# Kernel tuning notes

Measured on AMD Instinct MI355X. Metric: run time of the kernel, lower is better.

## Reference

```python
import jax, jax.numpy as jnp
import numpy as np

BASE_ALPHA = 0.05
NUM_ITER = 2
EPS = 1e-06


def setup_inputs() -> dict:
    key = jax.random.key(0)
    k1, k2 = jax.random.split(key)
    pred = jax.random.normal(k1, (8, 8192, 3), dtype=jnp.float32)
    partial = jax.random.normal(k2, (8, 2048, 3), dtype=jnp.float32)
    return {"pred": pred, "partial": partial}


def _cdist(a, b):
    # Euclidean pairwise distances via ||a||^2 - 2ab + ||b||^2 (avoids [B,N,M,3] temp).
    a2 = jnp.sum(a * a, axis=-1)  # [B,N]
    b2 = jnp.sum(b * b, axis=-1)  # [B,M]
    d2 = a2[:, :, None] - 2.0 * jnp.einsum('bnd,bmd->bnm', a, b) + b2[:, None, :]
    return jnp.sqrt(jnp.maximum(d2, 0.0))


def reference(pred, partial):
    refined = pred
    for _ in range(NUM_ITER):
        dist = _cdist(refined, partial)          # [B,N,M]
        min_dist = jnp.min(dist, axis=-1)        # [B,N]
        min_idx = jnp.argmin(dist, axis=-1)      # [B,N]
        nearest = jnp.take_along_axis(partial, min_idx[:, :, None], axis=1)  # [B,N,3]
        dist_norm = min_dist / (jnp.max(min_dist, axis=-1, keepdims=True) + EPS)
        alpha = BASE_ALPHA * (2.0 - dist_norm)   # [B,N]
        refined = refined + alpha[:, :, None] * (nearest - refined)
    return refined
```

## Files before the change

kernel.cpp:

```cpp
#include <hip/hip_runtime.h>
#include <math.h>

#define BATCH 8
#define NPRED 8192
#define MPART 2048
#define NPTS  (BATCH * NPRED)
#define MTOT  (BATCH * MPART)
#define QPL   4
#define SPLIT 16
#define PTS_PER_SPLIT (MPART / SPLIT)
#define GPS   (PTS_PER_SPLIT / 4)
#define QPB   256
#define NBLK  (NPTS / QPB)
#define BLK_PER_B (NPRED / QPB)
#define BASE_ALPHA 0.05f
#define EPS 1e-6f

typedef float fx16 __attribute__((ext_vector_type(16)));

__global__ __launch_bounds__(256) void prep_kernel(const float* __restrict__ partial,
                                                   float* __restrict__ ppgf,
                                                   float4* __restrict__ near4) {
    const int m = blockIdx.x * 256 + threadIdx.x;
    const float* p = partial + 3u * (unsigned)m;
    const float x = p[0], y = p[1], z = p[2];
    const int g = m >> 2, c = m & 3;
    float* base = ppgf + (size_t)g * 16 + c;
    base[0]  = -2.0f * x;
    base[4]  = -2.0f * y;
    base[8]  = -2.0f * z;
    base[12] = fmaf(x, x, fmaf(y, y, z * z));
    near4[m] = make_float4(x, y, z, 0.0f);
}

template <bool FUSE>
__global__ __launch_bounds__(1024) void nn_kernel(
    const float* __restrict__ src,
    const float4* __restrict__ ppg,
    const float4* __restrict__ near4,
    const float* md_in, const int* idx_in,
    const float* __restrict__ bmax_in,
    float* __restrict__ refined_out,
    float* md_out, int* idx_out,
    float* __restrict__ bmax_out)
{
    __shared__ unsigned long long lk[SPLIT * QPB];
    __shared__ float smax[4];

    const int qb   = blockIdx.x;
    const int b    = qb >> 5;
    const int tid  = threadIdx.x;
    const int wave = tid >> 6, lane = tid & 63;
    const int split = __builtin_amdgcn_readfirstlane(wave);

    float axq[QPL], ayq[QPL], azq[QPL], a2q[QPL];
    if (FUSE) {
        float v = bmax_in[(b << 5) + (lane & 31)];
        #pragma unroll
        for (int o = 32; o > 0; o >>= 1) v = fmaxf(v, __shfl_down(v, o, 64));
        const float maxv = __shfl(v, 0, 64);
        #pragma unroll
        for (int j = 0; j < QPL; ++j) {
            const int t = (qb << 8) + (j << 6) + lane;
            const float md = md_in[t];
            const int   id = idx_in[t];
            const float alpha = BASE_ALPHA * (2.0f - md / (maxv + EPS));
            const float4 nb = near4[((size_t)b << 11) + id];
            const float* p = src + 3u * (unsigned)t;
            const float px = p[0], py = p[1], pz = p[2];
            axq[j] = fmaf(alpha, nb.x - px, px);
            ayq[j] = fmaf(alpha, nb.y - py, py);
            azq[j] = fmaf(alpha, nb.z - pz, pz);
            if (split == 0) {
                float* o = refined_out + 3u * (unsigned)t;
                o[0] = axq[j]; o[1] = ayq[j]; o[2] = azq[j];
            }
        }
    } else {
        #pragma unroll
        for (int j = 0; j < QPL; ++j) {
            const int t = (qb << 8) + (j << 6) + lane;
            const float* p = src + 3u * (unsigned)t;
            axq[j] = p[0]; ayq[j] = p[1]; azq[j] = p[2];
        }
    }
    #pragma unroll
    for (int j = 0; j < QPL; ++j)
        a2q[j] = fmaf(axq[j], axq[j], fmaf(ayq[j], ayq[j], azq[j] * azq[j]));

    const fx16* gq = (const fx16*)(ppg + ((size_t)b << 11) + ((size_t)split << 7));

    float best[QPL]; int bg[QPL];
    #pragma unroll
    for (int j = 0; j < QPL; ++j) { best[j] = 1e30f; bg[j] = 0; }

    #pragma unroll 1
    for (int ii = 0; ii < GPS; ii += 2) {
        fx16 A, B;
        asm volatile("s_load_dwordx16 %0, %2, 0\n\t"
                     "s_load_dwordx16 %1, %2, 64"
                     : "=&s"(A), "=&s"(B)
                     : "s"(gq + ii));
        asm volatile("s_waitcnt lgkmcnt(0)" : "+s"(A), "+s"(B));

        #pragma unroll
        for (int j = 0; j < QPL; ++j) {
            const float ax = axq[j], ay = ayq[j], az = azq[j];
            const float d0 = fmaf(A[8],  az, fmaf(A[4], ay, A[0] * ax)) + A[12];
            const float d1 = fmaf(A[9],  az, fmaf(A[5], ay, A[1] * ax)) + A[13];
            const float d2 = fmaf(A[10], az, fmaf(A[6], ay, A[2] * ax)) + A[14];
            const float d3 = fmaf(A[11], az, fmaf(A[7], ay, A[3] * ax)) + A[15];
            const float gm = fminf(fminf(fminf(d0, d1), d2), d3);
            if (gm < best[j]) bg[j] = ii;
            best[j] = fminf(best[j], gm);
        }
        #pragma unroll
        for (int j = 0; j < QPL; ++j) {
            const float ax = axq[j], ay = ayq[j], az = azq[j];
            const float d0 = fmaf(B[8],  az, fmaf(B[4], ay, B[0] * ax)) + B[12];
            const float d1 = fmaf(B[9],  az, fmaf(B[5], ay, B[1] * ax)) + B[13];
            const float d2 = fmaf(B[10], az, fmaf(B[6], ay, B[2] * ax)) + B[14];
            const float d3 = fmaf(B[11], az, fmaf(B[7], ay, B[3] * ax)) + B[15];
            const float gm = fminf(fminf(fminf(d0, d1), d2), d3);
            if (gm < best[j]) bg[j] = ii + 1;
            best[j] = fminf(best[j], gm);
        }
    }

    const float4* wpg = ppg + ((size_t)b << 11) + ((size_t)split << 7);
    unsigned long long key[QPL];
    #pragma unroll
    for (int j = 0; j < QPL; ++j) {
        const int gi = bg[j];
        const float4 X = wpg[4 * gi + 0];
        const float4 Y = wpg[4 * gi + 1];
        const float4 Z = wpg[4 * gi + 2];
        const float4 W = wpg[4 * gi + 3];
        const float ax = axq[j], ay = ayq[j], az = azq[j];
        const float d0 = fmaf(Z.x, az, fmaf(Y.x, ay, X.x * ax)) + W.x;
        const float d1 = fmaf(Z.y, az, fmaf(Y.y, ay, X.y * ax)) + W.y;
        const float d2 = fmaf(Z.z, az, fmaf(Y.z, ay, X.z * ax)) + W.z;
        const float bv = best[j];
        int c;
        if      (d0 == bv) c = 0;
        else if (d1 == bv) c = 1;
        else if (d2 == bv) c = 2;
        else               c = 3;
        const int m = (split << 7) + (gi << 2) + c;
        const float dd = fmaxf(bv + a2q[j], 0.0f);
        key[j] = ((unsigned long long)__float_as_uint(dd) << 32) | (unsigned)m;
    }

    #pragma unroll
    for (int j = 0; j < QPL; ++j)
        lk[split * QPB + (j << 6) + lane] = key[j];
    __syncthreads();

    if (wave < 4) {
        const int q2 = (wave << 6) + lane;
        unsigned long long kk = lk[q2];
        #pragma unroll
        for (int s = 1; s < SPLIT; ++s) {
            const unsigned long long k = lk[s * QPB + q2];
            if (k < kk) kk = k;
        }
        const float md = sqrtf(__uint_as_float((unsigned)(kk >> 32)));
        const int t2 = (qb << 8) + q2;
        md_out[t2]  = md;
        idx_out[t2] = (int)(kk & 0xffffffffu);
        float w = md;
        #pragma unroll
        for (int o = 32; o > 0; o >>= 1) w = fmaxf(w, __shfl_down(w, o, 64));
        if (lane == 0) smax[wave] = w;
    }
    __syncthreads();
    if (tid == 0)
        bmax_out[qb] = fmaxf(fmaxf(smax[0], smax[1]), fmaxf(smax[2], smax[3]));
}

__global__ __launch_bounds__(256) void update_kernel(
    const float* __restrict__ refined1,
    const float4* __restrict__ near4,
    const float* __restrict__ md2,
    const int*   __restrict__ idx2,
    const float* __restrict__ bmax2,
    float* __restrict__ out)
{
    const int t = blockIdx.x * 256 + threadIdx.x;
    const int b = t >> 13;
    const int lane = threadIdx.x & 63;
    float v = bmax2[(b << 5) + (lane & 31)];
    #pragma unroll
    for (int o = 32; o > 0; o >>= 1) v = fmaxf(v, __shfl_down(v, o, 64));
    const float maxv = __shfl(v, 0, 64);
    const float md = md2[t];
    const int   id = idx2[t];
    const float alpha = BASE_ALPHA * (2.0f - md / (maxv + EPS));
    const float4 nb = near4[((size_t)b << 11) + id];
    const float* p = refined1 + 3u * (unsigned)t;
    const float px = p[0], py = p[1], pz = p[2];
    float* o = out + 3u * (unsigned)t;
    o[0] = fmaf(alpha, nb.x - px, px);
    o[1] = fmaf(alpha, nb.y - py, py);
    o[2] = fmaf(alpha, nb.z - pz, pz);
}

extern "C" void kernel_launch(void* const* d_in, const int* in_sizes, int n_in,
                              void* d_out, int out_size, void* d_ws, size_t ws_size,
                              hipStream_t stream) {
    const float* pred    = (const float*)d_in[0];
    const float* partial = (const float*)d_in[1];
    float* out = (float*)d_out;

    char* ws = (char*)d_ws;
    float4* ppg   = (float4*)ws;
    float4* near4 = (float4*)(ws + 262144);
    float*  ref1  = (float*)(ws + 524288);
    float*  md1   = (float*)(ws + 1310720);
    int*    idx1  = (int*)(ws + 1572864);
    float*  bmax1 = (float*)(ws + 1835008);
    float*  bmax2 = bmax1 + NBLK;

    prep_kernel<<<MTOT / 256, 256, 0, stream>>>(partial, (float*)ppg, near4);

    nn_kernel<false><<<NBLK, 1024, 0, stream>>>(
        pred, ppg, near4, nullptr, nullptr, nullptr, nullptr, md1, idx1, bmax1);

    nn_kernel<true><<<NBLK, 1024, 0, stream>>>(
        pred, ppg, near4, md1, idx1, bmax1, ref1, md1, idx1, bmax2);

    update_kernel<<<NPTS / 256, 256, 0, stream>>>(ref1, near4, md1, idx1, bmax2, out);
}
```

Baseline: 108.7 us.

## Stage partial-point groups in VGPRs and broadcast via readlane instead of scalar loads

Each wave now loads its 128 float4 partial-point entries once into two VGPRs per lane with vector loads. The fully unrolled scan then pulls the operands out with v_readlane into SGPRs, replacing the per-iteration s_load_dwordx16 pairs and their lgkmcnt waits. This is meant to remove scalar-memory latency stalls from the inner loop. In exchange it adds many readlane instructions, which may cost issue slots, and the full unroll of 32 groups increases code size.

```diff
diff --git a/kernel.cpp b/kernel.cpp
--- a/kernel.cpp
+++ b/kernel.cpp
@@ -12,11 +12,8 @@
 #define GPS   (PTS_PER_SPLIT / 4)
 #define QPB   256
 #define NBLK  (NPTS / QPB)
-#define BLK_PER_B (NPRED / QPB)
 #define BASE_ALPHA 0.05f
 #define EPS 1e-6f
-
-typedef float fx16 __attribute__((ext_vector_type(16)));
 
 __global__ __launch_bounds__(256) void prep_kernel(const float* __restrict__ partial,
                                                    float* __restrict__ ppgf,
@@ -33,6 +30,10 @@
     near4[m] = make_float4(x, y, z, 0.0f);
 }
 
+__device__ __forceinline__ float rlf(float v, int l) {
+    return __int_as_float(__builtin_amdgcn_readlane(__float_as_int(v), l));
+}
+
 template <bool FUSE>
 __global__ __launch_bounds__(1024) void nn_kernel(
     const float* __restrict__ src,
@@ -51,7 +52,11 @@
     const int b    = qb >> 5;
     const int tid  = threadIdx.x;
     const int wave = tid >> 6, lane = tid & 63;
-    const int split = __builtin_amdgcn_readfirstlane(wave);
+    const int split = wave;
+
+    const float4* wpg = ppg + ((size_t)b << 11) + ((size_t)split << 7);
+    const float4 t0 = wpg[lane];
+    const float4 t1 = wpg[64 + lane];
 
     float axq[QPL], ayq[QPL], azq[QPL], a2q[QPL];
     if (FUSE) {
@@ -88,46 +93,35 @@
     for (int j = 0; j < QPL; ++j)
         a2q[j] = fmaf(axq[j], axq[j], fmaf(ayq[j], ayq[j], azq[j] * azq[j]));
 
-    const fx16* gq = (const fx16*)(ppg + ((size_t)b << 11) + ((size_t)split << 7));
-
     float best[QPL]; int bg[QPL];
     #pragma unroll
     for (int j = 0; j < QPL; ++j) { best[j] = 1e30f; bg[j] = 0; }
 
-    #pragma unroll 1
-    for (int ii = 0; ii < GPS; ii += 2) {
-        fx16 A, B;
-        asm volatile("s_load_dwordx16 %0, %2, 0\n\t"
-                     "s_load_dwordx16 %1, %2, 64"
-                     : "=&s"(A), "=&s"(B)
-                     : "s"(gq + ii));
-        asm volatile("s_waitcnt lgkmcnt(0)" : "+s"(A), "+s"(B));
-
+    #pragma unroll
+    for (int i = 0; i < GPS; ++i) {
+        const float4 t = (i < 16) ? t0 : t1;
+        const int l0 = (i & 15) << 2;
+        const float Xx = rlf(t.x, l0 + 0), Xy = rlf(t.y, l0 + 0),
+                    Xz = rlf(t.z, l0 + 0), Xw = rlf(t.w, l0 + 0);
+        const float Yx = rlf(t.x, l0 + 1), Yy = rlf(t.y, l0 + 1),
+                    Yz = rlf(t.z, l0 + 1), Yw = rlf(t.w, l0 + 1);
+        const float Zx = rlf(t.x, l0 + 2), Zy = rlf(t.y, l0 + 2),
+                    Zz = rlf(t.z, l0 + 2), Zw = rlf(t.w, l0 + 2);
+        const float Wx = rlf(t.x, l0 + 3), Wy = rlf(t.y, l0 + 3),
+                    Wz = rlf(t.z, l0 + 3), Ww = rlf(t.w, l0 + 3);
         #pragma unroll
         for (int j = 0; j < QPL; ++j) {
             const float ax = axq[j], ay = ayq[j], az = azq[j];
-            const float d0 = fmaf(A[8],  az, fmaf(A[4], ay, A[0] * ax)) + A[12];
-            const float d1 = fmaf(A[9],  az, fmaf(A[5], ay, A[1] * ax)) + A[13];
-            const float d2 = fmaf(A[10], az, fmaf(A[6], ay, A[2] * ax)) + A[14];
-            const float d3 = fmaf(A[11], az, fmaf(A[7], ay, A[3] * ax)) + A[15];
+            const float d0 = fmaf(Zx, az, fmaf(Yx, ay, Xx * ax)) + Wx;
+            const float d1 = fmaf(Zy, az, fmaf(Yy, ay, Xy * ax)) + Wy;
+            const float d2 = fmaf(Zz, az, fmaf(Yz, ay, Xz * ax)) + Wz;
+            const float d3 = fmaf(Zw, az, fmaf(Yw, ay, Xw * ax)) + Ww;
             const float gm = fminf(fminf(fminf(d0, d1), d2), d3);
-            if (gm < best[j]) bg[j] = ii;
+            if (gm < best[j]) bg[j] = i;
             best[j] = fminf(best[j], gm);
         }
-        #pragma unroll
-        for (int j = 0; j < QPL; ++j) {
-            const float ax = axq[j], ay = ayq[j], az = azq[j];
-            const float d0 = fmaf(B[8],  az, fmaf(B[4], ay, B[0] * ax)) + B[12];
-            const float d1 = fmaf(B[9],  az, fmaf(B[5], ay, B[1] * ax)) + B[13];
-            const float d2 = fmaf(B[10], az, fmaf(B[6], ay, B[2] * ax)) + B[14];
-            const float d3 = fmaf(B[11], az, fmaf(B[7], ay, B[3] * ax)) + B[15];
-            const float gm = fminf(fminf(fminf(d0, d1), d2), d3);
-            if (gm < best[j]) bg[j] = ii + 1;
-            best[j] = fminf(best[j], gm);
-        }
-    }
-
-    const float4* wpg = ppg + ((size_t)b << 11) + ((size_t)split << 7);
+    }
+
     unsigned long long key[QPL];
     #pragma unroll
     for (int j = 0; j < QPL; ++j) {
```

Result: slower. 115.4 us (+6.2%).
